# Kernel tuning notes

Measured on AMD Instinct MI355X. Metric: run time of the kernel, lower is better.

The kernel has to match this reference:

```python
import jax, jax.numpy as jnp
import numpy as np

D_MODEL = 768
NUM_HEADS = 12
D_K = D_MODEL // NUM_HEADS


def setup_inputs() -> dict:
    key = jax.random.key(0)
    ks = jax.random.split(key, 12)
    B, S = 4, 2048
    s = 1.0 / np.sqrt(D_MODEL)
    inp = {
        "query": jax.random.normal(ks[0], (B, S, D_MODEL), jnp.float32),
        "key": jax.random.normal(ks[1], (B, S, D_MODEL), jnp.float32),
        "value": jax.random.normal(ks[2], (B, S, D_MODEL), jnp.float32),
        "Wq": jax.random.normal(ks[3], (D_MODEL, D_MODEL), jnp.float32) * s,
        "bq": jnp.zeros((D_MODEL,), jnp.float32),
        "Wk": jax.random.normal(ks[4], (D_MODEL, D_MODEL), jnp.float32) * s,
        "bk": jnp.zeros((D_MODEL,), jnp.float32),
        "Wv": jax.random.normal(ks[5], (D_MODEL, D_MODEL), jnp.float32) * s,
        "bv": jnp.zeros((D_MODEL,), jnp.float32),
        "Wo": jax.random.normal(ks[6], (D_MODEL, D_MODEL), jnp.float32) * s,
        "bo": jnp.zeros((D_MODEL,), jnp.float32),
    }
    return inp


def _split_heads(x):
    B, S, _ = x.shape
    return x.reshape(B, S, NUM_HEADS, D_K).transpose(0, 2, 1, 3)  # [B,H,S,Dk]


def reference(query, key, value, Wq, bq, Wk, bk, Wv, bv, Wo, bo):
    # Linear projections (torch nn.Linear: x @ W.T + b)
    Q = _split_heads(query @ Wq.T + bq)
    K = _split_heads(key @ Wk.T + bk)
    V = _split_heads(value @ Wv.T + bv)
    scale = 1.0 / jnp.sqrt(jnp.asarray(D_K, Q.dtype))
    scores = jnp.einsum("bhqd,bhkd->bhqk", Q, K) * scale  # [B,H,S,S]
    attn = jax.nn.softmax(scores, axis=-1)
    # dropout is identity in eval mode
    out = jnp.einsum("bhqk,bhkd->bhqd", attn, V)  # [B,H,S,Dk]
    B, H, S, Dk = out.shape
    out = out.transpose(0, 2, 1, 3).reshape(B, S, H * Dk)
    return out @ Wo.T + bo
```

## Files before the change

kernel.cpp:

```cpp
#include <hip/hip_runtime.h>
#include <hip/hip_bf16.h>

typedef _Float16 half8 __attribute__((ext_vector_type(8)));
typedef _Float16 h4 __attribute__((ext_vector_type(4)));
typedef __fp16 fp16x2 __attribute__((ext_vector_type(2)));
typedef float f32x4 __attribute__((ext_vector_type(4)));

#define D_MODEL 768
#define NUM_HEADS 12
#define D_K 64
#define SEQ 2048
#define BATCH 4
#define M_TOTAL (BATCH * SEQ)
#define W_ELEMS (D_MODEL * D_MODEL)
#define X_ELEMS (M_TOTAL * D_MODEL)
#define QSCALE 0.18033688011112042f
#define SOFF 4.0f

__device__ __forceinline__ void gll16(const _Float16* g, _Float16* l) {
    __builtin_amdgcn_global_load_lds(
        (const __attribute__((address_space(1))) unsigned int*)g,
        (__attribute__((address_space(3))) unsigned int*)l,
        16, 0, 0);
}

__global__ void convert_all(
    const float* __restrict__ w0, const float* __restrict__ w1,
    const float* __restrict__ w2, const float* __restrict__ w3,
    const float* __restrict__ x0, const float* __restrict__ x1,
    const float* __restrict__ x2, _Float16* __restrict__ dst)
{
    const size_t W4 = W_ELEMS / 4, X4 = X_ELEMS / 4;
    size_t i = (size_t)blockIdx.x * blockDim.x + threadIdx.x;
    const float* src;
    size_t off;
    if (i < 4 * W4) {
        size_t slab = i / W4;
        off = i - slab * W4;
        src = (slab == 0) ? w0 : (slab == 1) ? w1 : (slab == 2) ? w2 : w3;
    } else {
        size_t j = i - 4 * W4;
        size_t slab = j / X4;
        off = j - slab * X4;
        src = (slab == 0) ? x0 : (slab == 1) ? x1 : x2;
    }
    float4 f = ((const float4*)src)[off];
    h4 h;
    h[0] = (_Float16)f.x; h[1] = (_Float16)f.y;
    h[2] = (_Float16)f.z; h[3] = (_Float16)f.w;
    ((h4*)dst)[i] = h;
}

__global__ __launch_bounds__(256) void gemm_qkv(
    const _Float16* __restrict__ Xall, const _Float16* __restrict__ Wall,
    const float* __restrict__ bq, const float* __restrict__ bk, const float* __restrict__ bv,
    _Float16* __restrict__ Qo, _Float16* __restrict__ Ko, _Float16* __restrict__ Vto)
{
    __shared__ __align__(16) char smem[36864];
    _Float16* As = (_Float16*)smem;
    _Float16* Bs = As + 128 * 64;

    const int z = blockIdx.z;
    const _Float16* X = Xall + (size_t)z * X_ELEMS;
    const _Float16* W = Wall + (size_t)z * W_ELEMS;

    const int t = threadIdx.x;
    const int w = t >> 6;
    const int l = t & 63;
    const int ln = t & 15;
    const int quad = (t >> 4) & 3;
    const int wm = w >> 1, wn = w & 1;
    const int m0 = blockIdx.x * 128, n0 = blockIdx.y * 128;

    const int srow = l >> 3;
    const int scol = (l & 7) ^ srow;

    f32x4 acc[4][4] = {};

    for (int k0 = 0; k0 < D_MODEL; k0 += 64) {
#pragma unroll
        for (int jj = 0; jj < 4; ++jj) {
            int j = w * 4 + jj;
            int row = j * 8 + srow;
            gll16(X + (size_t)(m0 + row) * D_MODEL + k0 + scol * 8, As + j * 512);
            gll16(W + (size_t)(n0 + row) * D_MODEL + k0 + scol * 8, Bs + j * 512);
        }
        __syncthreads();

#pragma unroll
        for (int kk = 0; kk < 2; ++kk) {
            half8 a[4], b[4];
#pragma unroll
            for (int i = 0; i < 4; ++i) {
                int ra = wm * 64 + i * 16 + ln;
                int rb = wn * 64 + i * 16 + ln;
                a[i] = *(const half8*)&As[ra * 64 + (((kk * 4 + quad) ^ (ln & 7)) * 8)];
                b[i] = *(const half8*)&Bs[rb * 64 + (((kk * 4 + quad) ^ (ln & 7)) * 8)];
            }
            if (z <= 1) {
#pragma unroll
                for (int i = 0; i < 4; ++i)
#pragma unroll
                    for (int j2 = 0; j2 < 4; ++j2)
                        acc[i][j2] = __builtin_amdgcn_mfma_f32_16x16x32_f16(b[j2], a[i], acc[i][j2], 0, 0, 0);
            } else {
#pragma unroll
                for (int i = 0; i < 4; ++i)
#pragma unroll
                    for (int j2 = 0; j2 < 4; ++j2)
                        acc[i][j2] = __builtin_amdgcn_mfma_f32_16x16x32_f16(a[i], b[j2], acc[i][j2], 0, 0, 0);
            }
        }
        __syncthreads();
    }

    if (z <= 1) {
        const float* bias = (z == 0) ? bq : bk;
        _Float16* dst = (z == 0) ? Qo : Ko;
        const int head = (n0 + wn * 64) >> 6;
#pragma unroll
        for (int i = 0; i < 4; ++i) {
            int m = m0 + wm * 64 + i * 16 + ln;
            int b_ = m >> 11, s_ = m & 2047;
            _Float16* rowp = dst + ((size_t)((b_ * NUM_HEADS + head) * SEQ + s_)) * D_K;
#pragma unroll
            for (int j = 0; j < 4; ++j) {
                int dbase = j * 16 + quad * 4;
                f32x4 bn = *(const f32x4*)&bias[n0 + wn * 64 + dbase];
                h4 o;
#pragma unroll
                for (int r = 0; r < 4; ++r) {
                    float v = acc[i][j][r] + bn[r];
                    if (z == 0) v *= QSCALE;
                    o[r] = (_Float16)v;
                }
                *(h4*)&rowp[dbase] = o;
            }
        }
    } else {
        const float* bias = bv;
        _Float16* T = (_Float16*)smem + (size_t)w * (64 * 72);
#pragma unroll
        for (int i = 0; i < 4; ++i) {
#pragma unroll
            for (int j = 0; j < 4; ++j) {
                float bn = bias[n0 + wn * 64 + j * 16 + ln];
                h4 hh;
#pragma unroll
                for (int r = 0; r < 4; ++r) hh[r] = (_Float16)(acc[i][j][r] + bn);
                *(h4*)&T[(j * 16 + ln) * 72 + i * 16 + quad * 4] = hh;
            }
        }
        const int b_ = m0 >> 11;
        const int s0 = (m0 & 2047) + wm * 64;
        const int head = (n0 >> 6) + wn;
        _Float16* base = Vto + (size_t)(b_ * NUM_HEADS + head) * D_K * SEQ + s0;
        const int p = l & 7, tt = p >> 2, qq = p & 3;
#pragma unroll
        for (int r8 = 0; r8 < 8; ++r8) {
            int nl = r8 * 8 + (l >> 3);
            h4 lo = *(const h4*)&T[nl * 72 + tt * 32 + qq * 4];
            h4 hi = *(const h4*)&T[nl * 72 + tt * 32 + 16 + qq * 4];
            half8 v = __builtin_shufflevector(lo, hi, 0, 1, 2, 3, 4, 5, 6, 7);
            *(half8*)(base + (size_t)nl * SEQ + p * 8) = v;
        }
    }
}

__global__ __launch_bounds__(256, 3) void attn(
    const _Float16* __restrict__ Qg, const _Float16* __restrict__ Kg,
    const _Float16* __restrict__ Vtg, _Float16* __restrict__ ctx)
{
    __shared__ __align__(16) _Float16 Ks[2][64 * 64];
    __shared__ __align__(16) _Float16 Vs[2][64 * 64];

    const int t = threadIdx.x;
    const int w = t >> 6;
    const int l = t & 63;
    const int ln = t & 15;
    const int quad = (t >> 4) & 3;

    const int lid = blockIdx.x + (int)gridDim.x * blockIdx.y;
    const int nid = (lid & 7) * ((SEQ / 128) * (BATCH * NUM_HEADS) / 8) + (lid >> 3);
    const int bh = nid >> 4;
    const int q0 = (nid & 15) * 128 + w * 32;

    const _Float16* Qh = Qg + (size_t)bh * SEQ * D_K;
    const _Float16* Kh = Kg + (size_t)bh * SEQ * D_K;
    const _Float16* Vh = Vtg + (size_t)bh * D_K * SEQ;

    const int srow = l >> 3;
    const int scol = (l & 7) ^ srow;
    const _Float16* Ksrc0 = Kh + (size_t)(w * 16 + srow) * D_K + scol * 8;
    const _Float16* Ksrc1 = Kh + (size_t)(w * 16 + 8 + srow) * D_K + scol * 8;
    const _Float16* Vsrc0 = Vh + (size_t)(w * 16 + srow) * SEQ + scol * 8;
    const _Float16* Vsrc1 = Vh + (size_t)(w * 16 + 8 + srow) * SEQ + scol * 8;

    half8 qf[2][2];
#pragma unroll
    for (int qt = 0; qt < 2; ++qt)
#pragma unroll
        for (int dh = 0; dh < 2; ++dh)
            qf[qt][dh] = *(const half8*)(Qh + (size_t)(q0 + qt * 16 + ln) * D_K + dh * 32 + quad * 8);

    f32x4 acc[2][4] = {};
    f32x4 lsum[2] = {};
    f32x4 S[2][4];
    h4 pB[2][4];

    const int c0 = (quad ^ (ln & 7)) * 8;
    const int c1 = ((4 + quad) ^ (ln & 7)) * 8;

    auto stageK = [&](int c, int B) {
        const size_t koff = (size_t)c * 64 * D_K;
        gll16(Ksrc0 + koff, &Ks[B][w * 1024]);
        gll16(Ksrc1 + koff, &Ks[B][w * 1024 + 512]);
    };
    auto stageV = [&](int c, int B) {
        const size_t voff = (size_t)c * 64;
        gll16(Vsrc0 + voff, &Vs[B][w * 1024]);
        gll16(Vsrc1 + voff, &Vs[B][w * 1024 + 512]);
    };

    auto qk = [&](int B) {
        const _Float16* Ksc = Ks[B];
#pragma unroll
        for (int kt = 0; kt < 4; ++kt) {
            half8 kf0 = *(const half8*)&Ksc[(kt * 16 + ln) * 64 + c0];
            half8 kf1 = *(const half8*)&Ksc[(kt * 16 + ln) * 64 + c1];
#pragma unroll
            for (int qt = 0; qt < 2; ++qt) {
                f32x4 s = {-SOFF, -SOFF, -SOFF, -SOFF};
                s = __builtin_amdgcn_mfma_f32_16x16x32_f16(kf0, qf[qt][0], s, 0, 0, 0);
                s = __builtin_amdgcn_mfma_f32_16x16x32_f16(kf1, qf[qt][1], s, 0, 0, 0);
                S[qt][kt] = s;
            }
        }
    };

    auto smx = [&]() {
#pragma unroll
        for (int qt = 0; qt < 2; ++qt)
#pragma unroll
            for (int kt = 0; kt < 4; ++kt) {
                f32x4 s = S[qt][kt];
                f32x4 p;
                p[0] = __builtin_amdgcn_exp2f(s[0]);
                p[1] = __builtin_amdgcn_exp2f(s[1]);
                p[2] = __builtin_amdgcn_exp2f(s[2]);
                p[3] = __builtin_amdgcn_exp2f(s[3]);
                lsum[qt] += p;
                fp16x2 r0 = __builtin_amdgcn_cvt_pkrtz(p[0], p[1]);
                fp16x2 r1 = __builtin_amdgcn_cvt_pkrtz(p[2], p[3]);
                h4 h;
                h[0] = (_Float16)r0[0]; h[1] = (_Float16)r0[1];
                h[2] = (_Float16)r1[0]; h[3] = (_Float16)r1[1];
                pB[qt][kt] = h;
            }
    };

    auto pv = [&](int B) {
        const _Float16* Vsc = Vs[B];
        half8 pA0 = __builtin_shufflevector(pB[0][0], pB[0][1], 0, 1, 2, 3, 4, 5, 6, 7);
        half8 pA1 = __builtin_shufflevector(pB[0][2], pB[0][3], 0, 1, 2, 3, 4, 5, 6, 7);
        half8 pC0 = __builtin_shufflevector(pB[1][0], pB[1][1], 0, 1, 2, 3, 4, 5, 6, 7);
        half8 pC1 = __builtin_shufflevector(pB[1][2], pB[1][3], 0, 1, 2, 3, 4, 5, 6, 7);
        __builtin_amdgcn_s_setprio(1);
#pragma unroll
        for (int dt = 0; dt < 4; ++dt) {
            half8 va = *(const half8*)&Vsc[(dt * 16 + ln) * 64 + c0];
            half8 vb = *(const half8*)&Vsc[(dt * 16 + ln) * 64 + c1];
            acc[0][dt] = __builtin_amdgcn_mfma_f32_16x16x32_f16(va, pA0, acc[0][dt], 0, 0, 0);
            acc[0][dt] = __builtin_amdgcn_mfma_f32_16x16x32_f16(vb, pA1, acc[0][dt], 0, 0, 0);
            acc[1][dt] = __builtin_amdgcn_mfma_f32_16x16x32_f16(va, pC0, acc[1][dt], 0, 0, 0);
            acc[1][dt] = __builtin_amdgcn_mfma_f32_16x16x32_f16(vb, pC1, acc[1][dt], 0, 0, 0);
        }
        __builtin_amdgcn_s_setprio(0);
    };

    stageK(0, 0);
    stageK(1, 1);
    stageV(0, 0);
    asm volatile("s_waitcnt vmcnt(0)" ::: "memory");
    __builtin_amdgcn_s_barrier();
    qk(0);

    for (int c = 0; c < 31; ++c) {
        asm volatile("s_waitcnt vmcnt(0)" ::: "memory");
        __builtin_amdgcn_s_barrier();
        if (c < 30) stageK(c + 2, c & 1);
        stageV(c + 1, (c + 1) & 1);
        smx();
        qk((c + 1) & 1);
        pv(c & 1);
    }
    asm volatile("s_waitcnt vmcnt(0)" ::: "memory");
    __builtin_amdgcn_s_barrier();
    smx();
    pv(1);

    const int h = bh % NUM_HEADS, b = bh / NUM_HEADS;
#pragma unroll
    for (int qt = 0; qt < 2; ++qt) {
        float lp = lsum[qt][0] + lsum[qt][1] + lsum[qt][2] + lsum[qt][3];
        lp += __shfl_xor(lp, 16);
        lp += __shfl_xor(lp, 32);
        float rinv = __builtin_amdgcn_rcpf(lp);
        int q = q0 + qt * 16 + ln;
#pragma unroll
        for (int dt = 0; dt < 4; ++dt) {
            h4 o;
            o[0] = (_Float16)(acc[qt][dt][0] * rinv);
            o[1] = (_Float16)(acc[qt][dt][1] * rinv);
            o[2] = (_Float16)(acc[qt][dt][2] * rinv);
            o[3] = (_Float16)(acc[qt][dt][3] * rinv);
            *(h4*)&ctx[((size_t)(b * SEQ + q)) * D_MODEL + h * D_K + dt * 16 + quad * 4] = o;
        }
    }
}

__global__ __launch_bounds__(256) void gemm_out(
    const _Float16* __restrict__ A, const _Float16* __restrict__ W,
    const float* __restrict__ bo, float* __restrict__ out)
{
    __shared__ __align__(16) _Float16 As[128 * 64];
    __shared__ __align__(16) _Float16 Bs[64 * 64];

    const int t = threadIdx.x;
    const int w = t >> 6;
    const int l = t & 63;
    const int ln = t & 15;
    const int quad = (t >> 4) & 3;
    const int wm = w >> 1, wn = w & 1;
    const int m0 = blockIdx.x * 128, n0 = blockIdx.y * 64;

    const int srow = l >> 3;
    const int scol = (l & 7) ^ srow;

    f32x4 acc[4][2] = {};

    for (int k0 = 0; k0 < D_MODEL; k0 += 64) {
#pragma unroll
        for (int jj = 0; jj < 4; ++jj) {
            int j = w * 4 + jj;
            int row = j * 8 + srow;
            gll16(A + (size_t)(m0 + row) * D_MODEL + k0 + scol * 8, As + j * 512);
        }
#pragma unroll
        for (int jj = 0; jj < 2; ++jj) {
            int j = w * 2 + jj;
            int row = j * 8 + srow;
            gll16(W + (size_t)(n0 + row) * D_MODEL + k0 + scol * 8, Bs + j * 512);
        }
        __syncthreads();

#pragma unroll
        for (int kk = 0; kk < 2; ++kk) {
            half8 a[4], b[2];
#pragma unroll
            for (int i = 0; i < 4; ++i) {
                int ra = wm * 64 + i * 16 + ln;
                a[i] = *(const half8*)&As[ra * 64 + (((kk * 4 + quad) ^ (ln & 7)) * 8)];
            }
#pragma unroll
            for (int i = 0; i < 2; ++i) {
                int rb = wn * 32 + i * 16 + ln;
                b[i] = *(const half8*)&Bs[rb * 64 + (((kk * 4 + quad) ^ (ln & 7)) * 8)];
            }
#pragma unroll
            for (int i = 0; i < 4; ++i)
#pragma unroll
                for (int j2 = 0; j2 < 2; ++j2)
                    acc[i][j2] = __builtin_amdgcn_mfma_f32_16x16x32_f16(b[j2], a[i], acc[i][j2], 0, 0, 0);
        }
        __syncthreads();
    }

#pragma unroll
    for (int i = 0; i < 4; ++i) {
        int m = m0 + wm * 64 + i * 16 + ln;
        float* rowp = out + (size_t)m * D_MODEL;
#pragma unroll
        for (int j = 0; j < 2; ++j) {
            int nb = n0 + wn * 32 + j * 16 + quad * 4;
            f32x4 o = acc[i][j] + *(const f32x4*)&bo[nb];
            *(f32x4*)&rowp[nb] = o;
        }
    }
}

extern "C" void kernel_launch(void* const* d_in, const int* in_sizes, int n_in,
                              void* d_out, int out_size, void* d_ws, size_t ws_size,
                              hipStream_t stream) {
    const float* query = (const float*)d_in[0];
    const float* key   = (const float*)d_in[1];
    const float* value = (const float*)d_in[2];
    const float* Wq = (const float*)d_in[3];
    const float* bq = (const float*)d_in[4];
    const float* Wk = (const float*)d_in[5];
    const float* bk = (const float*)d_in[6];
    const float* Wv = (const float*)d_in[7];
    const float* bv = (const float*)d_in[8];
    const float* Wo = (const float*)d_in[9];
    const float* bo = (const float*)d_in[10];
    float* out = (float*)d_out;

    _Float16* ws = (_Float16*)d_ws;
    _Float16* Wb  = ws;
    _Float16* Xb  = Wb + 4 * (size_t)W_ELEMS;
    _Float16* Qb  = Xb + 3 * (size_t)X_ELEMS;
    _Float16* Kb  = Qb + (size_t)X_ELEMS;
    _Float16* Vtb = Kb + (size_t)X_ELEMS;
    _Float16* ctx = Vtb + (size_t)X_ELEMS;

    const size_t total4 = (4 * (size_t)W_ELEMS + 3 * (size_t)X_ELEMS) / 4;
    convert_all<<<(int)(total4 / 256), 256, 0, stream>>>(
        Wq, Wk, Wv, Wo, query, key, value, Wb);

    gemm_qkv<<<dim3(M_TOTAL / 128, D_MODEL / 128, 3), 256, 0, stream>>>(
        Xb, Wb, bq, bk, bv, Qb, Kb, Vtb);

    attn<<<dim3(SEQ / 128, BATCH * NUM_HEADS), 256, 0, stream>>>(Qb, Kb, Vtb, ctx);

    gemm_out<<<dim3(M_TOTAL / 128, D_MODEL / 64), 256, 0, stream>>>(
        ctx, Wb + 3 * (size_t)W_ELEMS, bo, out);
}
```

Baseline: 257.4 us.

## Remap GEMM blocks per XCD for L2 locality and widen fp16 conversion

Both projection GEMMs now decode the linear block id so that consecutive blocks dispatched to the same XCD (id mod 8) share the same group of M rows. All N tiles and QKV slabs for those rows stay within one XCD's L2. The aim is to cut redundant A-tile fetches across XCD caches. Separately, the fp32-to-fp16 conversion kernel now handles 8 elements per thread with 16-byte stores, halving the thread count. The remap relies on the grid dimensions dividing exactly, which holds for these fixed shapes.

```diff
diff --git a/kernel.cpp b/kernel.cpp
--- a/kernel.cpp
+++ b/kernel.cpp
@@ -30,25 +30,28 @@
     const float* __restrict__ x0, const float* __restrict__ x1,
     const float* __restrict__ x2, _Float16* __restrict__ dst)
 {
-    const size_t W4 = W_ELEMS / 4, X4 = X_ELEMS / 4;
+    const size_t W8 = W_ELEMS / 8, X8 = X_ELEMS / 8;
     size_t i = (size_t)blockIdx.x * blockDim.x + threadIdx.x;
     const float* src;
     size_t off;
-    if (i < 4 * W4) {
-        size_t slab = i / W4;
-        off = i - slab * W4;
+    if (i < 4 * W8) {
+        size_t slab = i / W8;
+        off = i - slab * W8;
         src = (slab == 0) ? w0 : (slab == 1) ? w1 : (slab == 2) ? w2 : w3;
     } else {
-        size_t j = i - 4 * W4;
-        size_t slab = j / X4;
-        off = j - slab * X4;
+        size_t j = i - 4 * W8;
+        size_t slab = j / X8;
+        off = j - slab * X8;
         src = (slab == 0) ? x0 : (slab == 1) ? x1 : x2;
     }
-    float4 f = ((const float4*)src)[off];
-    h4 h;
-    h[0] = (_Float16)f.x; h[1] = (_Float16)f.y;
-    h[2] = (_Float16)f.z; h[3] = (_Float16)f.w;
-    ((h4*)dst)[i] = h;
+    float4 f0 = ((const float4*)src)[off * 2];
+    float4 f1 = ((const float4*)src)[off * 2 + 1];
+    half8 h;
+    h[0] = (_Float16)f0.x; h[1] = (_Float16)f0.y;
+    h[2] = (_Float16)f0.z; h[3] = (_Float16)f0.w;
+    h[4] = (_Float16)f1.x; h[5] = (_Float16)f1.y;
+    h[6] = (_Float16)f1.z; h[7] = (_Float16)f1.w;
+    ((half8*)dst)[i] = h;
 }
 
 __global__ __launch_bounds__(256) void gemm_qkv(
@@ -60,7 +63,13 @@
     _Float16* As = (_Float16*)smem;
     _Float16* Bs = As + 128 * 64;
 
-    const int z = blockIdx.z;
+    const int lid = blockIdx.x + (int)gridDim.x * (blockIdx.y + (int)gridDim.y * blockIdx.z);
+    const int xcd = lid & 7, idx = lid >> 3;
+    const int mloc = idx / 18, rr = idx - mloc * 18;
+    const int z = rr / 6, nn = rr - (rr / 6) * 6;
+    const int m0 = (xcd * 8 + mloc) * 128;
+    const int n0 = nn * 128;
+
     const _Float16* X = Xall + (size_t)z * X_ELEMS;
     const _Float16* W = Wall + (size_t)z * W_ELEMS;
 
@@ -70,7 +79,6 @@
     const int ln = t & 15;
     const int quad = (t >> 4) & 3;
     const int wm = w >> 1, wn = w & 1;
-    const int m0 = blockIdx.x * 128, n0 = blockIdx.y * 128;
 
     const int srow = l >> 3;
     const int scol = (l & 7) ^ srow;
@@ -332,7 +340,12 @@
     const int ln = t & 15;
     const int quad = (t >> 4) & 3;
     const int wm = w >> 1, wn = w & 1;
-    const int m0 = blockIdx.x * 128, n0 = blockIdx.y * 64;
+
+    const int lid = blockIdx.x + (int)gridDim.x * blockIdx.y;
+    const int xcd = lid & 7, idx = lid >> 3;
+    const int mloc = idx / 12, nn = idx - mloc * 12;
+    const int m0 = (xcd * 8 + mloc) * 128;
+    const int n0 = nn * 64;
 
     const int srow = l >> 3;
     const int scol = (l & 7) ^ srow;
@@ -413,8 +426,8 @@
     _Float16* Vtb = Kb + (size_t)X_ELEMS;
     _Float16* ctx = Vtb + (size_t)X_ELEMS;
 
-    const size_t total4 = (4 * (size_t)W_ELEMS + 3 * (size_t)X_ELEMS) / 4;
-    convert_all<<<(int)(total4 / 256), 256, 0, stream>>>(
+    const size_t total8 = (4 * (size_t)W_ELEMS + 3 * (size_t)X_ELEMS) / 8;
+    convert_all<<<(int)(total8 / 256), 256, 0, stream>>>(
         Wq, Wk, Wv, Wo, query, key, value, Wb);
 
     gemm_qkv<<<dim3(M_TOTAL / 128, D_MODEL / 128, 3), 256, 0, stream>>>(
```

Result: no change. 258.7 us (+0.5%).
